# Optimization experiments

Measured on AMD Instinct MI355X. Metric: run time of the kernel, lower is better.

## Reference

```python
import jax, jax.numpy as jnp
import numpy as np


def _gcn_conv(x, src, dst, W, b, n):
    """PyG GCNConv with default settings: add self-loops, symmetric norm, bias after agg.
    out = D^{-1/2} (A + I) D^{-1/2} (x @ W) + b
    """
    h = x @ W  # [N, out]
    # degree of A+I with unit edge weights: 1 (self-loop) + in-degree on dst
    deg = jnp.ones((n,), x.dtype).at[dst].add(jnp.ones((dst.shape[0],), x.dtype))
    dinv = jax.lax.rsqrt(deg)  # [N]
    coef = dinv[src] * dinv[dst]  # [E]
    agg = jax.ops.segment_sum(h[src] * coef[:, None], dst, num_segments=n)
    # self-loop contribution: norm = dinv[i]*dinv[i]
    return agg + h * (dinv * dinv)[:, None] + b


def setup_inputs() -> dict:
    key = jax.random.key(0)
    ks = jax.random.split(key, 10)
    N, E, D, H1, H2 = 100000, 2500000, 128, 32, 64
    x = jax.random.normal(ks[0], (N, D), jnp.float32)
    ei = jax.random.randint(ks[1], (2, E), 0, N, dtype=jnp.int32)
    # GCN layer params (glorot-ish scale)
    W1c = jax.random.normal(ks[2], (D, H1), jnp.float32) / np.sqrt(D)
    b1c = jnp.zeros((H1,), jnp.float32)
    W2c = jax.random.normal(ks[3], (H1, H2), jnp.float32) / np.sqrt(H1)
    b2c = jnp.zeros((H2,), jnp.float32)
    # MLP head: Linear(H2,H2) -> ReLU -> Linear(H2,1)
    Wm1 = jax.random.normal(ks[4], (H2, H2), jnp.float32) / np.sqrt(H2)
    bm1 = jnp.zeros((H2,), jnp.float32)
    Wm2 = jax.random.normal(ks[5], (H2, 1), jnp.float32) / np.sqrt(H2)
    bm2 = jnp.zeros((1,), jnp.float32)
    return {"x": x, "W1c": W1c, "b1c": b1c, "W2c": W2c, "b2c": b2c,
            "Wm1": Wm1, "bm1": bm1, "Wm2": Wm2, "bm2": bm2,
            "ei": ei, "num_nodes": 50000}


def reference(x, W1c, b1c, W2c, b2c, Wm1, bm1, Wm2, bm2, ei, num_nodes):
    src, dst = ei[0], ei[1]
    n = x.shape[0]
    z = jax.nn.relu(_gcn_conv(x, src, dst, W1c, b1c, n))
    z = jax.nn.relu(_gcn_conv(z, src, dst, W2c, b2c, n))
    v = jax.nn.relu(z @ Wm1 + bm1) @ Wm2 + bm2  # [N, 1]
    nbatches = n // num_nodes
    # mean per-graph state value (reshape over stacked graphs, mean over nodes)
    return v.reshape(nbatches, num_nodes).mean(axis=1)
```

## Files before the change

### kernel.cpp

```cpp
#include <hip/hip_runtime.h>


typedef _Float16 half_t;
typedef __attribute__((ext_vector_type(8))) _Float16 half8;
typedef __attribute__((ext_vector_type(4))) float f32x4;
typedef __attribute__((ext_vector_type(2))) float f32x2;
typedef __attribute__((ext_vector_type(2))) int   i32x2;

#define CHUNK 8192
#define BKN   512
#define NBMAX 256

__global__ void k_zero_out(float* out, int n) {
    int i = blockIdx.x * blockDim.x + threadIdx.x;
    if (i < n) out[i] = 0.0f;
}


__global__ __launch_bounds__(256) void k_count_coarse(
    const int* __restrict__ dst, int* __restrict__ table, int E, int nblk, int NB)
{
    __shared__ int cnt[NBMAX];
    const int tid = threadIdx.x;
    for (int i = tid; i < NB; i += 256) cnt[i] = 0;
    __syncthreads();
    const int base = blockIdx.x * CHUNK;
    const int lim = min(CHUNK, E - base);
    if (lim == CHUNK) {
        const int4* d4 = (const int4*)(dst + base);
        for (int i = tid; i < CHUNK / 4; i += 256) {
            int4 v = d4[i];
            atomicAdd(&cnt[v.x >> 9], 1);
            atomicAdd(&cnt[v.y >> 9], 1);
            atomicAdd(&cnt[v.z >> 9], 1);
            atomicAdd(&cnt[v.w >> 9], 1);
        }
    } else {
        for (int i = tid; i < lim; i += 256) atomicAdd(&cnt[dst[base + i] >> 9], 1);
    }
    __syncthreads();
    for (int b = tid; b < NB; b += 256) table[b * nblk + blockIdx.x] = cnt[b];
}

__global__ __launch_bounds__(256) void k_scan1(const int* __restrict__ cnts, int* __restrict__ S,
                                               int* __restrict__ bsums, int T) {
    __shared__ int sh[256];
    int t = threadIdx.x;
    int i = blockIdx.x * 256 + t;
    int v = (i < T) ? cnts[i] : 0;
    sh[t] = v;
    __syncthreads();
    for (int off = 1; off < 256; off <<= 1) {
        int tv = (t >= off) ? sh[t - off] : 0;
        __syncthreads();
        sh[t] += tv;
        __syncthreads();
    }
    if (i < T) S[i + 1] = sh[t];
    if (t == 255) bsums[blockIdx.x] = sh[255];
}

__global__ __launch_bounds__(1024) void k_scan2(int* bs, int nb) {
    __shared__ int sh[1024];
    int t = threadIdx.x;
    int v = (t < nb) ? bs[t] : 0;
    sh[t] = v;
    __syncthreads();
    for (int off = 1; off < 1024; off <<= 1) {
        int tv = (t >= off) ? sh[t - off] : 0;
        __syncthreads();
        sh[t] += tv;
        __syncthreads();
    }
    if (t < nb) bs[t] = sh[t] - v;
}

__global__ void k_scan3(int* __restrict__ S, const int* __restrict__ bs, int T) {
    int i = blockIdx.x * blockDim.x + threadIdx.x;
    if (i < T) S[i + 1] += bs[i >> 8];
    if (i == 0) S[0] = 0;
}

__global__ __launch_bounds__(256) void k_scatter2(
    const int* __restrict__ ei, const int* __restrict__ S,
    int* __restrict__ codes, int E, int nblk, int NB)
{
    __shared__ int cur[NBMAX];
    const int tid = threadIdx.x;
    for (int i = tid; i < NB; i += 256) cur[i] = S[i * nblk + blockIdx.x];
    __syncthreads();
    const int base = blockIdx.x * CHUNK;
    const int lim = min(CHUNK, E - base);
    if (lim == CHUNK) {
        const int4* s4 = (const int4*)(ei + base);
        const int4* d4 = (const int4*)(ei + E + base);
        for (int i = tid; i < CHUNK / 4; i += 256) {
            int4 sv = s4[i], dv = d4[i];
            { int pos = atomicAdd(&cur[dv.x >> 9], 1); codes[pos] = ((dv.x & 511) << 17) | sv.x; }
            { int pos = atomicAdd(&cur[dv.y >> 9], 1); codes[pos] = ((dv.y & 511) << 17) | sv.y; }
            { int pos = atomicAdd(&cur[dv.z >> 9], 1); codes[pos] = ((dv.z & 511) << 17) | sv.z; }
            { int pos = atomicAdd(&cur[dv.w >> 9], 1); codes[pos] = ((dv.w & 511) << 17) | sv.w; }
        }
    } else {
        for (int i = tid; i < lim; i += 256) {
            int e = base + i;
            int s = ei[e], d = ei[E + e];
            int pos = atomicAdd(&cur[d >> 9], 1);
            codes[pos] = ((d & 511) << 17) | s;
        }
    }
}

__global__ __launch_bounds__(512) void k_fine(
    const int* __restrict__ codes, const int* __restrict__ S,
    int* __restrict__ esrc, int* __restrict__ row_start,
    float* __restrict__ dinv, int nblk, int N, int E, int NB)
{
    __shared__ int cnt[BKN];
    __shared__ int sh[BKN];
    __shared__ int cur[BKN];
    const int tid = threadIdx.x;
    cnt[tid] = 0;
    __syncthreads();
    const int b = blockIdx.x;
    const int beg = S[b * nblk], end = S[(b + 1) * nblk];
    for (int e = beg + tid; e < end; e += 512) atomicAdd(&cnt[codes[e] >> 17], 1);
    __syncthreads();
    sh[tid] = cnt[tid];
    __syncthreads();
    for (int off = 1; off < 512; off <<= 1) {
        int tv = (tid >= off) ? sh[tid - off] : 0;
        __syncthreads();
        sh[tid] += tv;
        __syncthreads();
    }
    {
        int fs = beg + sh[tid] - cnt[tid];
        cur[tid] = fs;
        int n = b * BKN + tid;
        if (n < N) {
            row_start[n] = fs;
            dinv[n] = rsqrtf(1.0f + (float)cnt[tid]);
        }
    }
    if (b == NB - 1 && tid == 0) row_start[N] = E;
    __syncthreads();
    for (int e = beg + tid; e < end; e += 512) {
        int c = codes[e];
        int pos = atomicAdd(&cur[c >> 17], 1);
        esrc[pos] = c & 0x1FFFF;
    }
}


__global__ __launch_bounds__(256) void k_prep(
    const float* __restrict__ W1, const float* __restrict__ W2, const float* __restrict__ Wm1,
    half_t* __restrict__ W1t, half_t* __restrict__ W2t, half_t* __restrict__ Wm1t,
    float* __restrict__ out, int out_n)
{
    int i = blockIdx.x * 256 + threadIdx.x;
    if (i < 128 * 32) { int k = i >> 5, c = i & 31; W1t[c * 128 + k] = (half_t)W1[i]; }
    if (i < 32 * 64)  { int k = i >> 6, c = i & 63; W2t[c * 32 + k]  = (half_t)W2[i]; }
    if (i < 64 * 64)  { int k = i >> 6, c = i & 63; Wm1t[c * 64 + k] = (half_t)Wm1[i]; }
    if (i < out_n) out[i] = 0.0f;
}

__global__ __launch_bounds__(256) void k_gemm1_mfma(
    const float* __restrict__ x, const half_t* __restrict__ W1t,
    const float* __restrict__ dinv, unsigned char* __restrict__ hs8, int N)
{
    const int tid = threadIdx.x;
    const int wid = tid >> 6, lane = tid & 63;
    const int quad = lane >> 4, n16 = lane & 15;
    const int n0 = blockIdx.x * 64 + wid * 16;
    if (n0 >= N) return;
    const int nrow = min(n0 + n16, N - 1);
    const float* xr = x + (size_t)nrow * 128;
    f32x4 acc0 = {0.f, 0.f, 0.f, 0.f}, acc1 = {0.f, 0.f, 0.f, 0.f};
#pragma unroll
    for (int kc = 0; kc < 4; ++kc) {
        float4 f0 = *(const float4*)(xr + kc * 32 + quad * 8);
        float4 f1 = *(const float4*)(xr + kc * 32 + quad * 8 + 4);
        half8 a;
        a[0] = (half_t)f0.x; a[1] = (half_t)f0.y; a[2] = (half_t)f0.z; a[3] = (half_t)f0.w;
        a[4] = (half_t)f1.x; a[5] = (half_t)f1.y; a[6] = (half_t)f1.z; a[7] = (half_t)f1.w;
        half8 b0 = *(const half8*)(W1t + (size_t)n16 * 128 + kc * 32 + quad * 8);
        half8 b1 = *(const half8*)(W1t + (size_t)(16 + n16) * 128 + kc * 32 + quad * 8);
        acc0 = __builtin_amdgcn_mfma_f32_16x16x32_f16(a, b0, acc0, 0, 0, 0);
        acc1 = __builtin_amdgcn_mfma_f32_16x16x32_f16(a, b1, acc1, 0, 0, 0);
    }
#pragma unroll
    for (int r = 0; r < 4; ++r) {
        int n = n0 + quad * 4 + r;
        if (n < N) {
            float dv = dinv[n];
            int w0 = __builtin_amdgcn_cvt_pk_fp8_f32(acc0[r] * dv, 0.f, 0, false);
            int w1 = __builtin_amdgcn_cvt_pk_fp8_f32(acc1[r] * dv, 0.f, 0, false);
            hs8[(size_t)n * 32 + n16]      = (unsigned char)(w0 & 0xFF);
            hs8[(size_t)n * 32 + 16 + n16] = (unsigned char)(w1 & 0xFF);
        }
    }
}

__device__ __forceinline__ void unpack_acc8(i32x2 w, float* acc) {
    f32x2 p;
    p = __builtin_amdgcn_cvt_pk_f32_fp8(w.x, false); acc[0] += p.x; acc[1] += p.y;
    p = __builtin_amdgcn_cvt_pk_f32_fp8(w.x, true);  acc[2] += p.x; acc[3] += p.y;
    p = __builtin_amdgcn_cvt_pk_f32_fp8(w.y, false); acc[4] += p.x; acc[5] += p.y;
    p = __builtin_amdgcn_cvt_pk_f32_fp8(w.y, true);  acc[6] += p.x; acc[7] += p.y;
}

template <bool L1>
__global__ __launch_bounds__(256) void k_agg8(
    const int* __restrict__ row_start, const int* __restrict__ esrc,
    const int* __restrict__ IN, const float* __restrict__ bias,
    const float* __restrict__ dinv, void* __restrict__ OUT, int N)
{
    const int tid = threadIdx.x;
    const int g = tid >> 2, l = tid & 3;
    const int n = blockIdx.x * 64 + g;
    if (n >= N) return;
    const int beg = row_start[n], end = row_start[n + 1];
    float acc[8] = {0.f, 0.f, 0.f, 0.f, 0.f, 0.f, 0.f, 0.f};
    {
        i32x2 ws_ = *(const i32x2*)(IN + (size_t)n * 8 + l * 2);
        unpack_acc8(ws_, acc);
    }
    int e = beg;
    for (; e + 3 < end; e += 4) {
        int s0 = __builtin_nontemporal_load(esrc + e);
        int s1 = __builtin_nontemporal_load(esrc + e + 1);
        int s2 = __builtin_nontemporal_load(esrc + e + 2);
        int s3 = __builtin_nontemporal_load(esrc + e + 3);
        i32x2 w0 = *(const i32x2*)(IN + (size_t)s0 * 8 + l * 2);
        i32x2 w1 = *(const i32x2*)(IN + (size_t)s1 * 8 + l * 2);
        i32x2 w2 = *(const i32x2*)(IN + (size_t)s2 * 8 + l * 2);
        i32x2 w3 = *(const i32x2*)(IN + (size_t)s3 * 8 + l * 2);
        unpack_acc8(w0, acc);
        unpack_acc8(w1, acc);
        unpack_acc8(w2, acc);
        unpack_acc8(w3, acc);
    }
    for (; e < end; ++e) {
        int s = __builtin_nontemporal_load(esrc + e);
        i32x2 w = *(const i32x2*)(IN + (size_t)s * 8 + l * 2);
        unpack_acc8(w, acc);
    }
    const float dv = dinv[n];
    if (L1) {
        float v[8];
#pragma unroll
        for (int j = 0; j < 8; ++j)
            v[j] = fmaxf(dv * acc[j] + bias[l * 8 + j], 0.f) * dv;
        int o0 = __builtin_amdgcn_cvt_pk_fp8_f32(v[0], v[1], 0, false);
        o0     = __builtin_amdgcn_cvt_pk_fp8_f32(v[2], v[3], o0, true);
        int o1 = __builtin_amdgcn_cvt_pk_fp8_f32(v[4], v[5], 0, false);
        o1     = __builtin_amdgcn_cvt_pk_fp8_f32(v[6], v[7], o1, true);
        i32x2 ov = {o0, o1};
        __builtin_nontemporal_store(ov, (i32x2*)((int*)OUT + (size_t)n * 8 + l * 2));
    } else {
        half8 o;
#pragma unroll
        for (int j = 0; j < 8; ++j) o[j] = (half_t)(dv * acc[j]);
        __builtin_nontemporal_store(o, (half8*)((half_t*)OUT + (size_t)n * 32 + l * 8));
    }
}

__global__ __launch_bounds__(256) void k_tail_mfma(
    const half_t* __restrict__ Y, const half_t* __restrict__ W2t, const float* __restrict__ b2,
    const half_t* __restrict__ Wm1t, const float* __restrict__ bm1,
    const float* __restrict__ Wm2, const float* __restrict__ bm2,
    const int* __restrict__ nn_p, float* __restrict__ out, int N, int n_graphs)
{
    __shared__ float gacc[32];
    __shared__ __align__(16) half_t Hb[4][16][72];
    const int tid = threadIdx.x;
    if (tid < 32) gacc[tid] = 0.f;
    __syncthreads();
    const int wid = tid >> 6, lane = tid & 63;
    const int quad = lane >> 4, n16 = lane & 15;
    const int n0 = blockIdx.x * 64 + wid * 16;
    if (n0 < N) {
        const int nrow = min(n0 + n16, N - 1);
        half8 a1 = *(const half8*)(Y + (size_t)nrow * 32 + quad * 8);
        f32x4 acc1[4];
#pragma unroll
        for (int t = 0; t < 4; ++t) {
            half8 bf = *(const half8*)(W2t + (size_t)(t * 16 + n16) * 32 + quad * 8);
            f32x4 z = {0.f, 0.f, 0.f, 0.f};
            acc1[t] = __builtin_amdgcn_mfma_f32_16x16x32_f16(a1, bf, z, 0, 0, 0);
        }
#pragma unroll
        for (int t = 0; t < 4; ++t) {
            int c = t * 16 + n16;
            float bb = b2[c];
#pragma unroll
            for (int r = 0; r < 4; ++r)
                Hb[wid][quad * 4 + r][c] = (half_t)fmaxf(acc1[t][r] + bb, 0.f);
        }
        half8 a2lo = *(const half8*)&Hb[wid][n16][quad * 8];
        half8 a2hi = *(const half8*)&Hb[wid][n16][32 + quad * 8];
        f32x4 acc2[4];
#pragma unroll
        for (int t = 0; t < 4; ++t) {
            half8 b0 = *(const half8*)(Wm1t + (size_t)(t * 16 + n16) * 64 + quad * 8);
            half8 b1 = *(const half8*)(Wm1t + (size_t)(t * 16 + n16) * 64 + 32 + quad * 8);
            f32x4 a = {0.f, 0.f, 0.f, 0.f};
            a = __builtin_amdgcn_mfma_f32_16x16x32_f16(a2lo, b0, a, 0, 0, 0);
            a = __builtin_amdgcn_mfma_f32_16x16x32_f16(a2hi, b1, a, 0, 0, 0);
            acc2[t] = a;
        }
        float vsum[4] = {0.f, 0.f, 0.f, 0.f};
#pragma unroll
        for (int t = 0; t < 4; ++t) {
            int c = t * 16 + n16;
            float bb = bm1[c], ww = Wm2[c];
#pragma unroll
            for (int r = 0; r < 4; ++r)
                vsum[r] += fmaxf(acc2[t][r] + bb, 0.f) * ww;
        }
#pragma unroll
        for (int m = 1; m < 16; m <<= 1) {
#pragma unroll
            for (int r = 0; r < 4; ++r) vsum[r] += __shfl_xor(vsum[r], m, 64);
        }
        if (n16 == 0) {
            const int nnv = nn_p[0];
            const float bm2v = bm2[0];
#pragma unroll
            for (int r = 0; r < 4; ++r) {
                int n = n0 + quad * 4 + r;
                if (n < N) {
                    int g = n / nnv;
                    if (g < 32) atomicAdd(&gacc[g], vsum[r] + bm2v);
                }
            }
        }
    }
    __syncthreads();
    if (tid < n_graphs && tid < 32) atomicAdd(&out[tid], gacc[tid] / (float)nn_p[0]);
}

__global__ void k_zero_int(int* p, int n) {
    int i = blockIdx.x * blockDim.x + threadIdx.x;
    if (i < n) p[i] = 0;
}
__global__ void k_hist(const int* __restrict__ dst, int* __restrict__ deg, int E) {
    int e = blockIdx.x * blockDim.x + threadIdx.x;
    if (e < E) atomicAdd(&deg[dst[e]], 1);
}
__global__ void k_dinv(const int* __restrict__ deg, float* __restrict__ dinv, int n) {
    int i = blockIdx.x * blockDim.x + threadIdx.x;
    if (i < n) dinv[i] = rsqrtf(1.0f + (float)deg[i]);
}
__global__ __launch_bounds__(256) void k_gemm1f(
    const float* __restrict__ x, const float* __restrict__ W,
    const float* __restrict__ dinv, float* __restrict__ hs1, int N)
{
    __shared__ float Wl[128 * 32];
    __shared__ __align__(16) float Xl[8 * 132];
    const int tid = threadIdx.x;
    for (int i = tid; i < 128 * 32; i += 256) Wl[i] = W[i];
    const int node0 = blockIdx.x * 8;
    {
        int r = tid >> 5, c4 = tid & 31;
        int node = node0 + r;
        float4 v = make_float4(0.f, 0.f, 0.f, 0.f);
        if (node < N) v = ((const float4*)(x + (size_t)node * 128))[c4];
        *(float4*)&Xl[r * 132 + c4 * 4] = v;
    }
    __syncthreads();
    const int row = tid >> 5, f = tid & 31;
    float acc = 0.f;
#pragma unroll
    for (int k = 0; k < 128; k += 4) {
        float4 xv = *(const float4*)&Xl[row * 132 + k];
        acc += xv.x * Wl[(k + 0) * 32 + f];
        acc += xv.y * Wl[(k + 1) * 32 + f];
        acc += xv.z * Wl[(k + 2) * 32 + f];
        acc += xv.w * Wl[(k + 3) * 32 + f];
    }
    const int node = node0 + row;
    if (node < N) hs1[(size_t)node * 32 + f] = acc * dinv[node];
}
__global__ __launch_bounds__(256) void k_gemm2(
    const float* __restrict__ agg1, const float* __restrict__ W,
    const float* __restrict__ dinv, float* __restrict__ hs2, int N)
{
    __shared__ float Wl[32 * 64];
    __shared__ __align__(16) float Zl[4 * 36];
    const int tid = threadIdx.x;
    for (int i = tid; i < 32 * 64; i += 256) Wl[i] = W[i];
    const int node0 = blockIdx.x * 4;
    if (tid < 128) {
        int r = tid >> 5, c = tid & 31;
        int node = node0 + r;
        float v = 0.f;
        if (node < N) v = fmaxf(agg1[(size_t)node * 32 + c], 0.f);
        Zl[r * 36 + c] = v;
    }
    __syncthreads();
    const int row = tid >> 6, f = tid & 63;
    float acc = 0.f;
#pragma unroll
    for (int k = 0; k < 32; k += 4) {
        float4 zv = *(const float4*)&Zl[row * 36 + k];
        acc += zv.x * Wl[(k + 0) * 64 + f];
        acc += zv.y * Wl[(k + 1) * 64 + f];
        acc += zv.z * Wl[(k + 2) * 64 + f];
        acc += zv.w * Wl[(k + 3) * 64 + f];
    }
    int node = node0 + row;
    if (node < N) hs2[(size_t)node * 64 + f] = acc * dinv[node];
}
template <int F>
__global__ void k_agg_init(const float* __restrict__ hs, const float* __restrict__ b,
                           const float* __restrict__ dinv, float* __restrict__ agg, int N)
{
    long long t = (long long)blockIdx.x * blockDim.x + threadIdx.x;
    int n = (int)(t / F), f = (int)(t % F);
    if (n < N) agg[(size_t)n * F + f] = hs[(size_t)n * F + f] * dinv[n] + b[f];
}
template <int F>
__global__ void k_edge_atomic(const int* __restrict__ ei, const float* __restrict__ hs,
                              const float* __restrict__ dinv, float* __restrict__ agg, int E)
{
    long long tid = (long long)blockIdx.x * blockDim.x + threadIdx.x;
    int e = (int)(tid / F), f = (int)(tid % F);
    if (e < E) {
        int s = ei[e], d = ei[E + e];
        atomicAdd(&agg[(size_t)d * F + f], hs[(size_t)s * F + f] * dinv[d]);
    }
}
__global__ __launch_bounds__(256) void k_mlp(
    const float* __restrict__ agg2, const float* __restrict__ Wm1,
    const float* __restrict__ bm1, const float* __restrict__ Wm2,
    const float* __restrict__ bm2, float* __restrict__ vout, int N)
{
    __shared__ float Wl[64 * 64];
    __shared__ float W2l[64];
    __shared__ __align__(16) float Zl[4][64];
    const int tid = threadIdx.x;
    for (int i = tid; i < 64 * 64; i += 256) Wl[i] = Wm1[i];
    if (tid < 64) W2l[tid] = Wm2[tid];
    const int wid = tid >> 6, lane = tid & 63;
    const int node = blockIdx.x * 4 + wid;
    float zv = 0.f;
    if (node < N) zv = fmaxf(agg2[(size_t)node * 64 + lane], 0.f);
    Zl[wid][lane] = zv;
    __syncthreads();
    float t = bm1[lane];
#pragma unroll
    for (int k = 0; k < 64; k += 4) {
        float4 z4 = *(const float4*)&Zl[wid][k];
        t += z4.x * Wl[(k + 0) * 64 + lane];
        t += z4.y * Wl[(k + 1) * 64 + lane];
        t += z4.z * Wl[(k + 2) * 64 + lane];
        t += z4.w * Wl[(k + 3) * 64 + lane];
    }
    t = fmaxf(t, 0.f);
    float val = t * W2l[lane];
#pragma unroll
    for (int off = 32; off > 0; off >>= 1) val += __shfl_down(val, off, 64);
    if (lane == 0 && node < N) vout[node] = val + bm2[0];
}
__global__ void k_reduce(const float* __restrict__ v, const int* __restrict__ num_nodes_p,
                         float* out, int N, int n_graphs)
{
    __shared__ float acc[32];
    int tid = threadIdx.x;
    if (tid < n_graphs) acc[tid] = 0.f;
    __syncthreads();
    int i = blockIdx.x * blockDim.x + tid;
    int nn = num_nodes_p[0];
    if (i < N) {
        int g = i / nn;
        if (g < n_graphs) atomicAdd(&acc[g], v[i]);
    }
    __syncthreads();
    if (tid < n_graphs) atomicAdd(&out[tid], acc[tid] / (float)nn);
}

extern "C" void kernel_launch(void* const* d_in, const int* in_sizes, int n_in,
                              void* d_out, int out_size, void* d_ws, size_t ws_size,
                              hipStream_t stream)
{
    const float* x   = (const float*)d_in[0];
    const float* W1  = (const float*)d_in[1];
    const float* b1  = (const float*)d_in[2];
    const float* W2  = (const float*)d_in[3];
    const float* b2  = (const float*)d_in[4];
    const float* Wm1 = (const float*)d_in[5];
    const float* bm1 = (const float*)d_in[6];
    const float* Wm2 = (const float*)d_in[7];
    const float* bm2 = (const float*)d_in[8];
    const int*   ei  = (const int*)d_in[9];
    const int*   nn  = (const int*)d_in[10];
    const int N = in_sizes[0] / 128;
    const int E = in_sizes[9] / 2;
    float* out = (float*)d_out;

    const int NB = (N + BKN - 1) / BKN;
    const int nblk = (E + CHUNK - 1) / CHUNK;
    const long long T = (long long)NB * nblk;
    const int nb1 = (int)((T + 255) / 256);
    auto al4 = [](size_t v) { return (v + 3) & ~(size_t)3; };
    const size_t need_ints = al4(T) + al4(T + 1) + 1024 + al4(E) + al4(E)
                           + al4(N + 1) + al4(N) + 8ull * N + 8ull * N
                           + 16ull * N + 5120 + 64;
    const bool use_new = (N <= 131072) && (T <= 262144) && (nb1 <= 1024)
                       && (NB <= NBMAX) && (out_size <= 32)
                       && (ws_size >= need_ints * sizeof(int));

    if (use_new) {
        int* w = (int*)d_ws;
        int*    table     = w;                          w += al4(T);
        int*    S         = w;                          w += al4(T + 1);
        int*    bsums     = w;                          w += 1024;
        int*    codes     = w;                          w += al4(E);
        int*    esrc      = w;                          w += al4(E);
        int*    row_start = w;                          w += al4(N + 1);
        float*  dinv      = (float*)w;                  w += al4(N);
        int*    hs8       = w;                          w += 8ull * N;
        int*    Zs8       = w;                          w += 8ull * N;
        half_t* Y         = (half_t*)w;                 w += 16ull * N;
        half_t* W1t       = (half_t*)w;
        half_t* W2t       = W1t + 4096;
        half_t* Wm1t      = W2t + 2048;
        const int agrid = (N + 63) / 64;

        k_count_coarse<<<nblk, 256, 0, stream>>>(ei + E, table, E, nblk, NB);
        k_scan1<<<nb1, 256, 0, stream>>>(table, S, bsums, (int)T);
        k_scan2<<<1, 1024, 0, stream>>>(bsums, nb1);
        k_scan3<<<nb1, 256, 0, stream>>>(S, bsums, (int)T);
        k_scatter2<<<nblk, 256, 0, stream>>>(ei, S, codes, E, nblk, NB);
        k_fine<<<NB, 512, 0, stream>>>(codes, S, esrc, row_start, dinv, nblk, N, E, NB);
        k_prep<<<16, 256, 0, stream>>>(W1, W2, Wm1, W1t, W2t, Wm1t, out, out_size);
        k_gemm1_mfma<<<agrid, 256, 0, stream>>>(x, W1t, dinv, (unsigned char*)hs8, N);
        k_agg8<true><<<agrid, 256, 0, stream>>>(row_start, esrc, hs8, b1, dinv, Zs8, N);
        k_agg8<false><<<agrid, 256, 0, stream>>>(row_start, esrc, Zs8, b1, dinv, Y, N);
        k_tail_mfma<<<agrid, 256, 0, stream>>>(Y, W2t, b2, Wm1t, bm1, Wm2, bm2,
                                               nn, out, N, out_size);
    } else {
        const size_t Ns = (size_t)N;
        float* dinv = (float*)d_ws;
        float* B    = dinv + N;
        float* hs1  = B;
        float* agg1 = B + 32 * Ns;
        float* hs2  = B + 64 * Ns;
        float* agg2 = B + 128 * Ns;
        float* vtmp = B;
        int*   deg  = (int*)B;

        const int nb = (N + 255) / 256;
        k_zero_out<<<1, 64, 0, stream>>>(out, out_size);
        k_zero_int<<<nb, 256, 0, stream>>>(deg, N);
        k_hist<<<(E + 255) / 256, 256, 0, stream>>>(ei + E, deg, E);
        k_dinv<<<nb, 256, 0, stream>>>(deg, dinv, N);
        k_gemm1f<<<(N + 7) / 8, 256, 0, stream>>>(x, W1, dinv, hs1, N);
        {
            long long t = (long long)N * 32;
            k_agg_init<32><<<(unsigned)((t + 255) / 256), 256, 0, stream>>>(hs1, b1, dinv, agg1, N);
            t = (long long)E * 32;
            k_edge_atomic<32><<<(unsigned)((t + 255) / 256), 256, 0, stream>>>(ei, hs1, dinv, agg1, E);
        }
        k_gemm2<<<(N + 3) / 4, 256, 0, stream>>>(agg1, W2, dinv, hs2, N);
        {
            long long t = (long long)N * 64;
            k_agg_init<64><<<(unsigned)((t + 255) / 256), 256, 0, stream>>>(hs2, b2, dinv, agg2, N);
            t = (long long)E * 64;
            k_edge_atomic<64><<<(unsigned)((t + 255) / 256), 256, 0, stream>>>(ei, hs2, dinv, agg2, E);
        }
        k_mlp<<<(N + 3) / 4, 256, 0, stream>>>(agg2, Wm1, bm1, Wm2, bm2, vtmp, N);
        k_reduce<<<nb, 256, 0, stream>>>(vtmp, nn, out, N, out_size);
    }
}
```

Baseline: 262.4 us.

## Fuse layer-2 aggregation into MLP tail, drop scan3, halve sort chunk

The second aggregation now writes its fp16 rows into shared memory inside the tail MFMA kernel, so the global Y buffer round-trip and one kernel launch go away. The scan3 fix-up kernel is removed, and consumers add the block sums on the fly when they read S. CHUNK drops from 8192 to 4096, which doubles the number of coarse blocks and the size of the scan table. In exchange, the tail kernel now carries the irregular gather work, and the larger table adds scan cost.

Result: faster. 245.3 us (-6.5%).

```diff
diff --git a/kernel.cpp b/kernel.cpp
--- a/kernel.cpp
+++ b/kernel.cpp
@@ -7,13 +7,17 @@
 typedef __attribute__((ext_vector_type(2))) float f32x2;
 typedef __attribute__((ext_vector_type(2))) int   i32x2;
 
-#define CHUNK 8192
+#define CHUNK 4096
 #define BKN   512
 #define NBMAX 256
 
 __global__ void k_zero_out(float* out, int n) {
     int i = blockIdx.x * blockDim.x + threadIdx.x;
     if (i < n) out[i] = 0.0f;
+}
+
+__device__ __forceinline__ int sfull(const int* S, const int* bs, int j) {
+    return (j == 0) ? 0 : S[j] + bs[(j - 1) >> 8];
 }
 
 
@@ -75,19 +79,14 @@
     if (t < nb) bs[t] = sh[t] - v;
 }
 
-__global__ void k_scan3(int* __restrict__ S, const int* __restrict__ bs, int T) {
-    int i = blockIdx.x * blockDim.x + threadIdx.x;
-    if (i < T) S[i + 1] += bs[i >> 8];
-    if (i == 0) S[0] = 0;
-}
-
 __global__ __launch_bounds__(256) void k_scatter2(
-    const int* __restrict__ ei, const int* __restrict__ S,
+    const int* __restrict__ ei, const int* __restrict__ S, const int* __restrict__ bsums,
     int* __restrict__ codes, int E, int nblk, int NB)
 {
     __shared__ int cur[NBMAX];
     const int tid = threadIdx.x;
-    for (int i = tid; i < NB; i += 256) cur[i] = S[i * nblk + blockIdx.x];
+    for (int i = tid; i < NB; i += 256)
+        cur[i] = sfull(S, bsums, i * nblk + blockIdx.x);
     __syncthreads();
     const int base = blockIdx.x * CHUNK;
     const int lim = min(CHUNK, E - base);
@@ -112,7 +111,7 @@
 }
 
 __global__ __launch_bounds__(512) void k_fine(
-    const int* __restrict__ codes, const int* __restrict__ S,
+    const int* __restrict__ codes, const int* __restrict__ S, const int* __restrict__ bsums,
     int* __restrict__ esrc, int* __restrict__ row_start,
     float* __restrict__ dinv, int nblk, int N, int E, int NB)
 {
@@ -123,7 +122,7 @@
     cnt[tid] = 0;
     __syncthreads();
     const int b = blockIdx.x;
-    const int beg = S[b * nblk], end = S[(b + 1) * nblk];
+    const int beg = sfull(S, bsums, b * nblk), end = sfull(S, bsums, (b + 1) * nblk);
     for (int e = beg + tid; e < end; e += 512) atomicAdd(&cnt[codes[e] >> 17], 1);
     __syncthreads();
     sh[tid] = cnt[tid];
@@ -210,18 +209,11 @@
     p = __builtin_amdgcn_cvt_pk_f32_fp8(w.y, true);  acc[6] += p.x; acc[7] += p.y;
 }
 
-template <bool L1>
-__global__ __launch_bounds__(256) void k_agg8(
+__device__ __forceinline__ void gather_row8(
     const int* __restrict__ row_start, const int* __restrict__ esrc,
-    const int* __restrict__ IN, const float* __restrict__ bias,
-    const float* __restrict__ dinv, void* __restrict__ OUT, int N)
-{
-    const int tid = threadIdx.x;
-    const int g = tid >> 2, l = tid & 3;
-    const int n = blockIdx.x * 64 + g;
-    if (n >= N) return;
+    const int* __restrict__ IN, int n, int l, float* acc)
+{
     const int beg = row_start[n], end = row_start[n + 1];
-    float acc[8] = {0.f, 0.f, 0.f, 0.f, 0.f, 0.f, 0.f, 0.f};
     {
         i32x2 ws_ = *(const i32x2*)(IN + (size_t)n * 8 + l * 2);
         unpack_acc8(ws_, acc);
@@ -246,43 +238,65 @@
         i32x2 w = *(const i32x2*)(IN + (size_t)s * 8 + l * 2);
         unpack_acc8(w, acc);
     }
+}
+
+__global__ __launch_bounds__(256) void k_agg8_l1(
+    const int* __restrict__ row_start, const int* __restrict__ esrc,
+    const int* __restrict__ IN, const float* __restrict__ bias,
+    const float* __restrict__ dinv, int* __restrict__ OUT, int N)
+{
+    const int tid = threadIdx.x;
+    const int g = tid >> 2, l = tid & 3;
+    const int n = blockIdx.x * 64 + g;
+    if (n >= N) return;
+    float acc[8] = {0.f, 0.f, 0.f, 0.f, 0.f, 0.f, 0.f, 0.f};
+    gather_row8(row_start, esrc, IN, n, l, acc);
     const float dv = dinv[n];
-    if (L1) {
-        float v[8];
-#pragma unroll
-        for (int j = 0; j < 8; ++j)
-            v[j] = fmaxf(dv * acc[j] + bias[l * 8 + j], 0.f) * dv;
-        int o0 = __builtin_amdgcn_cvt_pk_fp8_f32(v[0], v[1], 0, false);
-        o0     = __builtin_amdgcn_cvt_pk_fp8_f32(v[2], v[3], o0, true);
-        int o1 = __builtin_amdgcn_cvt_pk_fp8_f32(v[4], v[5], 0, false);
-        o1     = __builtin_amdgcn_cvt_pk_fp8_f32(v[6], v[7], o1, true);
-        i32x2 ov = {o0, o1};
-        __builtin_nontemporal_store(ov, (i32x2*)((int*)OUT + (size_t)n * 8 + l * 2));
-    } else {
-        half8 o;
-#pragma unroll
-        for (int j = 0; j < 8; ++j) o[j] = (half_t)(dv * acc[j]);
-        __builtin_nontemporal_store(o, (half8*)((half_t*)OUT + (size_t)n * 32 + l * 8));
-    }
-}
-
-__global__ __launch_bounds__(256) void k_tail_mfma(
-    const half_t* __restrict__ Y, const half_t* __restrict__ W2t, const float* __restrict__ b2,
+    float v[8];
+#pragma unroll
+    for (int j = 0; j < 8; ++j)
+        v[j] = fmaxf(dv * acc[j] + bias[l * 8 + j], 0.f) * dv;
+    int o0 = __builtin_amdgcn_cvt_pk_fp8_f32(v[0], v[1], 0, false);
+    o0     = __builtin_amdgcn_cvt_pk_fp8_f32(v[2], v[3], o0, true);
+    int o1 = __builtin_amdgcn_cvt_pk_fp8_f32(v[4], v[5], 0, false);
+    o1     = __builtin_amdgcn_cvt_pk_fp8_f32(v[6], v[7], o1, true);
+    i32x2 ov = {o0, o1};
+    __builtin_nontemporal_store(ov, (i32x2*)(OUT + (size_t)n * 8 + l * 2));
+}
+
+__global__ __launch_bounds__(256) void k_agg8_tail(
+    const int* __restrict__ row_start, const int* __restrict__ esrc,
+    const int* __restrict__ IN, const float* __restrict__ dinv,
+    const half_t* __restrict__ W2t, const float* __restrict__ b2,
     const half_t* __restrict__ Wm1t, const float* __restrict__ bm1,
     const float* __restrict__ Wm2, const float* __restrict__ bm2,
     const int* __restrict__ nn_p, float* __restrict__ out, int N, int n_graphs)
 {
     __shared__ float gacc[32];
+    __shared__ __align__(16) half_t Yb[64][40];
     __shared__ __align__(16) half_t Hb[4][16][72];
     const int tid = threadIdx.x;
     if (tid < 32) gacc[tid] = 0.f;
+    {
+        const int g = tid >> 2, l = tid & 3;
+        const int n = blockIdx.x * 64 + g;
+        if (n < N) {
+            float acc[8] = {0.f, 0.f, 0.f, 0.f, 0.f, 0.f, 0.f, 0.f};
+            gather_row8(row_start, esrc, IN, n, l, acc);
+            const float dv = dinv[n];
+#pragma unroll
+            for (int j = 0; j < 8; ++j) Yb[g][l * 8 + j] = (half_t)(dv * acc[j]);
+        } else {
+#pragma unroll
+            for (int j = 0; j < 8; ++j) Yb[g][l * 8 + j] = (half_t)0.f;
+        }
+    }
     __syncthreads();
     const int wid = tid >> 6, lane = tid & 63;
     const int quad = lane >> 4, n16 = lane & 15;
     const int n0 = blockIdx.x * 64 + wid * 16;
     if (n0 < N) {
-        const int nrow = min(n0 + n16, N - 1);
-        half8 a1 = *(const half8*)(Y + (size_t)nrow * 32 + quad * 8);
+        half8 a1 = *(const half8*)&Yb[wid * 16 + n16][quad * 8];
         f32x4 acc1[4];
 #pragma unroll
         for (int t = 0; t < 4; ++t) {
@@ -507,7 +521,7 @@
     auto al4 = [](size_t v) { return (v + 3) & ~(size_t)3; };
     const size_t need_ints = al4(T) + al4(T + 1) + 1024 + al4(E) + al4(E)
                            + al4(N + 1) + al4(N) + 8ull * N + 8ull * N
-                           + 16ull * N + 5120 + 64;
+                           + 5120 + 64;
     const bool use_new = (N <= 131072) && (T <= 262144) && (nb1 <= 1024)
                        && (NB <= NBMAX) && (out_size <= 32)
                        && (ws_size >= need_ints * sizeof(int));
@@ -523,7 +537,6 @@
         float*  dinv      = (float*)w;                  w += al4(N);
         int*    hs8       = w;                          w += 8ull * N;
         int*    Zs8       = w;                          w += 8ull * N;
-        half_t* Y         = (half_t*)w;                 w += 16ull * N;
         half_t* W1t       = (half_t*)w;
         half_t* W2t       = W1t + 4096;
         half_t* Wm1t      = W2t + 2048;
@@ -532,14 +545,13 @@
         k_count_coarse<<<nblk, 256, 0, stream>>>(ei + E, table, E, nblk, NB);
         k_scan1<<<nb1, 256, 0, stream>>>(table, S, bsums, (int)T);
         k_scan2<<<1, 1024, 0, stream>>>(bsums, nb1);
-        k_scan3<<<nb1, 256, 0, stream>>>(S, bsums, (int)T);
-        k_scatter2<<<nblk, 256, 0, stream>>>(ei, S, codes, E, nblk, NB);
-        k_fine<<<NB, 512, 0, stream>>>(codes, S, esrc, row_start, dinv, nblk, N, E, NB);
+        k_scatter2<<<nblk, 256, 0, stream>>>(ei, S, bsums, codes, E, nblk, NB);
+        k_fine<<<NB, 512, 0, stream>>>(codes, S, bsums, esrc, row_start, dinv, nblk, N, E, NB);
         k_prep<<<16, 256, 0, stream>>>(W1, W2, Wm1, W1t, W2t, Wm1t, out, out_size);
         k_gemm1_mfma<<<agrid, 256, 0, stream>>>(x, W1t, dinv, (unsigned char*)hs8, N);
-        k_agg8<true><<<agrid, 256, 0, stream>>>(row_start, esrc, hs8, b1, dinv, Zs8, N);
-        k_agg8<false><<<agrid, 256, 0, stream>>>(row_start, esrc, Zs8, b1, dinv, Y, N);
-        k_tail_mfma<<<agrid, 256, 0, stream>>>(Y, W2t, b2, Wm1t, bm1, Wm2, bm2,
+        k_agg8_l1<<<agrid, 256, 0, stream>>>(row_start, esrc, hs8, b1, dinv, Zs8, N);
+        k_agg8_tail<<<agrid, 256, 0, stream>>>(row_start, esrc, Zs8, dinv,
+                                               W2t, b2, Wm1t, bm1, Wm2, bm2,
                                                nn, out, N, out_size);
     } else {
         const size_t Ns = (size_t)N;
```
